# Performance work log

Measured on AMD Instinct MI355X. Metric: run time of the kernel, lower is better.

The kernel has to match this reference:

```python
import jax, jax.numpy as jnp
import numpy as np

B, NEG, NBR, NS, D, T, E = 1024, 5, 50, 1000000, 128, 8, 4
NORM_RATE = 1e-4
NEG_INF = -2.0 ** 32 + 1.0


def leaky(x):
    return jax.nn.leaky_relu(x, 0.01)


def g(x, y):
    # negative squared L2 distance over last dim
    return -jnp.sum((x - y) ** 2, axis=-1)


def setup_inputs():
    key = jax.random.key(0)
    k = jax.random.split(key, 24)
    r_e = float(np.sqrt(3.0 / (NS + D)))
    r_t = float(np.sqrt(3.0 / (D + D)))
    return {
        'e_types': jax.random.randint(k[0], (B,), 0, E),
        's_ids': jax.random.randint(k[1], (B,), 0, NS),
        's_types': jax.random.randint(k[2], (B,), 0, T),
        's_negs': jax.random.randint(k[3], (B, NEG), 0, NS),
        's_nbr_ids': jax.random.randint(k[4], (E, B, NBR), 0, NS),
        's_nbr_masks': jax.random.randint(k[5], (E, B, NBR), 0, 2, dtype=jnp.int32),
        's_nbr_weights': jax.random.uniform(k[6], (E, B, NBR)),
        's_nbr_flags': jax.random.randint(k[7], (E, B, 1), 0, 2, dtype=jnp.int32),
        't_ids': jax.random.randint(k[8], (B,), 0, NS),
        't_types': jax.random.randint(k[9], (B,), 0, T),
        't_negs': jax.random.randint(k[10], (B, NEG), 0, NS),
        't_nbr_ids': jax.random.randint(k[11], (E, B, NBR), 0, NS),
        't_nbr_masks': jax.random.randint(k[12], (E, B, NBR), 0, 2, dtype=jnp.int32),
        't_nbr_weights': jax.random.uniform(k[13], (E, B, NBR)),
        't_nbr_flags': jax.random.randint(k[14], (E, B, 1), 0, 2, dtype=jnp.int32),
        'embedding': jax.random.uniform(k[15], (NS, D), minval=-r_e, maxval=r_e),
        'edge_type_embed': jax.random.uniform(k[16], (E, D), minval=-r_t, maxval=r_t),
        'W_node': jax.random.normal(k[17], (D, D)) * 0.05,
        'b_node': jnp.zeros((D,)),
        'W_nbr': jax.random.normal(k[18], (D, D)) * 0.05,
        'b_nbr': jnp.zeros((D,)),
        'W_att': jax.random.normal(k[19], (D, 1)) * 0.05,
        'b_att': jnp.zeros((1,)),
    }


def _node_latent(emb, W, b, ids):
    # scatter into [n*T, D] then gather at the same unique indices == identity,
    # so this reduces to a gathered linear + leaky_relu.
    return leaky(emb[ids] @ W + b)


def _edge_dist(node_e, ids, e_emb, weight, mask_i, target_e, negs, emb, Wn, bn, Wa, ba):
    # node_e [B,D], ids/weight/mask [B,N], e_emb [D], target_e [B,D], negs [neg,B,D]\n
    mask = mask_i.astype(bool)
    nbr = leaky(emb[ids] @ Wn + bn)                          # [B,N,D]
    d = g(node_e[:, None] + e_emb, nbr)                      # [B,N]
    atts = jax.nn.softmax(jnp.where(mask, d, NEG_INF), axis=-1)
    atts2 = jnp.where(mask, atts, 0.0)
    nw = atts2 * weight                                      # [B,N]
    mutual = g(nbr, target_e[:, None])                       # [B,N]
    mneg = jax.vmap(lambda ne: g(nbr, ne[:, None]))(negs)    # [neg,B,N]
    avg_embed = jnp.einsum('bn,bnd->bd', atts2, nbr)
    nbr_n = jnp.clip(jnp.sum(mask_i.astype(jnp.float32), 1), 1.0, float(NBR))
    ave_w = jnp.sum(weight, 1) / nbr_n                       # [B]
    hete = leaky((ave_w[:, None] * avg_embed) @ Wa + ba)     # [B,1]
    pos = jnp.sum(nw * mutual, -1)                           # [B]
    neg = jnp.sum(nw[None] * mneg, -1)                       # [neg,B]
    return pos, jnp.transpose(neg), hete[:, 0]


def _mutual(node_e, nbr_ids, nbr_masks, nbr_weights, nbr_flags, target_e, negs, emb, ete, Wn, bn, Wa, ba):
    pos, neg, hete = jax.vmap(
        _edge_dist,
        in_axes=(None, 0, 0, 0, 0, None, None, None, None, None, None, None),
    )(node_e, nbr_ids, ete, nbr_weights, nbr_masks, target_e, negs, emb, Wn, bn, Wa, ba)
    # original zeroes the per-type outputs when all flags > 0
    allpos = jnp.all(nbr_flags > 0, axis=(1, 2))             # [E]
    pos = jnp.where(allpos[:, None], 0.0, pos)               # [E,B]
    neg = jnp.where(allpos[:, None, None], 0.0, neg)         # [E,B,neg]
    hete = jnp.where(allpos[:, None], 0.0, hete)             # [E,B]
    mask_et = jnp.transpose(nbr_flags[:, :, 0] > 0)          # [B,E]
    att = jnp.transpose(hete)                                # [B,E]
    att_v1 = jax.nn.softmax(jnp.where(mask_et, att, NEG_INF), axis=1)
    norm_att = jax.nn.softmax(jnp.where(mask_et, att_v1, 0.0), axis=1)
    pos_loss = jnp.sum(norm_att * jnp.transpose(pos), axis=-1)            # [B]
    neg_loss = jnp.einsum('bne,be->bn', jnp.transpose(neg, (1, 2, 0)), norm_att)  # [B,neg]
    return pos_loss, neg_loss


def _forward(e_types, s_ids, s_negs, s_nbr_ids, s_nbr_masks, s_nbr_weights, s_nbr_flags,
             t_ids, t_negs, t_nbr_ids, t_nbr_masks, t_nbr_weights, t_nbr_flags,
             embedding, ete, Wn, bn, Wb, bb, Wa, ba):
    s_e = _node_latent(embedding, Wn, bn, s_ids)             # [B,D]
    t_e = _node_latent(embedding, Wn, bn, t_ids)
    mu = g(s_e + ete[e_types], t_e)                          # [B]
    neg_t = _node_latent(embedding, Wn, bn, t_negs)          # [B,neg,D]
    neg_s = _node_latent(embedding, Wn, bn, s_negs)
    neg_mus_st = g(s_e[:, None], neg_t)                      # [B,neg]
    neg_mus_ts = g(t_e[:, None], neg_s)
    pos_st, neg_st = _mutual(s_e, s_nbr_ids, s_nbr_masks, s_nbr_weights, s_nbr_flags,
                             t_e, jnp.transpose(neg_t, (1, 0, 2)), embedding, ete, Wb, bb, Wa, ba)
    pos_ts, neg_ts = _mutual(t_e, t_nbr_ids, t_nbr_masks, t_nbr_weights, t_nbr_flags,
                             s_e, jnp.transpose(neg_s, (1, 0, 2)), embedding, ete, Wb, bb, Wa, ba)
    lam_pos = mu + pos_st + pos_ts
    loss = (-jnp.mean(jnp.log(jax.nn.sigmoid(lam_pos) + 1e-6))
            - jnp.mean(jnp.log(jax.nn.sigmoid(-(neg_mus_st + neg_st)) + 1e-6))
            - jnp.mean(jnp.log(jax.nn.sigmoid(-(neg_mus_ts + neg_ts)) + 1e-6))
            + NORM_RATE * jnp.sum(ete ** 2))
    return loss


def reference(e_types, s_ids, s_types, s_negs, s_nbr_ids, s_nbr_masks, s_nbr_weights, s_nbr_flags,
              t_ids, t_types, t_negs, t_nbr_ids, t_nbr_masks, t_nbr_weights, t_nbr_flags,
              embedding, edge_type_embed, W_node, b_node, W_nbr, b_nbr, W_att, b_att):
    # s_types/t_types are mathematically inert (scatter/gather cancels); kept for signature fidelity.
    return _forward(e_types, s_ids, s_negs, s_nbr_ids, s_nbr_masks, s_nbr_weights, s_nbr_flags,
                    t_ids, t_negs, t_nbr_ids, t_nbr_masks, t_nbr_weights, t_nbr_flags,
                    embedding, edge_type_embed, W_node, b_node, W_nbr, b_nbr, W_att, b_att)
```

## Files before the change

### kernel.cpp

```cpp
#include <hip/hip_runtime.h>
#include <hip/hip_bf16.h>
#include <cstddef>

#define BN   1024
#define NEGN 5
#define NBRN 50
#define DN   128
#define EN   4
#define MPAD 64
#define NEG_INF_F (-4294967295.0f)

typedef __bf16 bf16_t;
typedef __bf16 bf16x8 __attribute__((ext_vector_type(8)));
typedef __bf16 bf16x4 __attribute__((ext_vector_type(4)));
typedef float  f32x4  __attribute__((ext_vector_type(4)));

__device__ __forceinline__ float leaky_f(float x) { return x >= 0.0f ? x : 0.01f * x; }

__device__ __forceinline__ float wave_sum(float v) {
#pragma unroll
    for (int off = 32; off; off >>= 1) v += __shfl_xor(v, off, 64);
    return v;
}
__device__ __forceinline__ float wave_max(float v) {
#pragma unroll
    for (int off = 32; off; off >>= 1) v = fmaxf(v, __shfl_xor(v, off, 64));
    return v;
}
__device__ __forceinline__ float sigmoid_f(float x) {
    if (x >= 0.0f) { float z = __expf(-x); return 1.0f / (1.0f + z); }
    float z = __expf(x); return z / (1.0f + z);
}

__global__ __launch_bounds__(256) void prep_kernel(
    const float* __restrict__ Wn, bf16_t* __restrict__ WnT)
{
    const int idx = blockIdx.x * 256 + threadIdx.x;
    if (idx < DN * DN) {
        const int n = idx >> 7, k = idx & 127;
        WnT[idx] = (bf16_t)Wn[k * DN + n];
    }
}

__global__ __launch_bounds__(128) void latent_kernel(
    const float* __restrict__ emb, const float* __restrict__ W, const float* __restrict__ bias,
    const int* __restrict__ s_ids, const int* __restrict__ t_ids,
    const int* __restrict__ s_negs, const int* __restrict__ t_negs,
    float* __restrict__ sE, float* __restrict__ tE,
    float* __restrict__ negS, float* __restrict__ negT)
{
    const int tid = threadIdx.x;
    const int r0 = blockIdx.x * 8;
    __shared__ float rows[8][DN];
    __shared__ int ids_l[8];

    if (tid < 8) {
        int r = r0 + tid;
        int id;
        if (r < BN)                       id = s_ids[r];
        else if (r < 2 * BN)              id = t_ids[r - BN];
        else if (r < 2 * BN + BN * NEGN)  id = s_negs[r - 2 * BN];
        else                              id = t_negs[r - 2 * BN - BN * NEGN];
        ids_l[tid] = id;
    }
    __syncthreads();
#pragma unroll
    for (int r8 = 0; r8 < 8; ++r8)
        rows[r8][tid] = emb[(size_t)ids_l[r8] * DN + tid];
    __syncthreads();

    float acc[8];
#pragma unroll
    for (int r8 = 0; r8 < 8; ++r8) acc[r8] = 0.0f;

    for (int i0 = 0; i0 < DN; i0 += 4) {
        const float w0 = W[(i0 + 0) * DN + tid];
        const float w1 = W[(i0 + 1) * DN + tid];
        const float w2 = W[(i0 + 2) * DN + tid];
        const float w3 = W[(i0 + 3) * DN + tid];
#pragma unroll
        for (int r8 = 0; r8 < 8; ++r8) {
            const float4 a = *reinterpret_cast<const float4*>(&rows[r8][i0]);
            acc[r8] = fmaf(a.x, w0, fmaf(a.y, w1, fmaf(a.z, w2, fmaf(a.w, w3, acc[r8]))));
        }
    }
    const float bb = bias[tid];
#pragma unroll
    for (int r8 = 0; r8 < 8; ++r8) {
        const int r = r0 + r8;
        const float v = leaky_f(acc[r8] + bb);
        float* dst;
        if (r < BN)                       dst = sE   + (size_t)r * DN;
        else if (r < 2 * BN)              dst = tE   + (size_t)(r - BN) * DN;
        else if (r < 2 * BN + BN * NEGN)  dst = negS + (size_t)(r - 2 * BN) * DN;
        else                              dst = negT + (size_t)(r - 2 * BN - BN * NEGN) * DN;
        dst[tid] = v;
    }
}

__global__ __launch_bounds__(256, 4) void edge_kernel(
    const float* __restrict__ emb, const float* __restrict__ ete,
    const bf16_t* __restrict__ WnT, const float* __restrict__ bn,
    const float* __restrict__ Wa, const float* __restrict__ ba,
    const int* __restrict__ s_nbr_ids, const int* __restrict__ s_nbr_masks, const float* __restrict__ s_nbr_w,
    const int* __restrict__ t_nbr_ids, const int* __restrict__ t_nbr_masks, const float* __restrict__ t_nbr_w,
    const float* __restrict__ sE, const float* __restrict__ tE,
    const float* __restrict__ negS, const float* __restrict__ negT,
    float* __restrict__ posW, float* __restrict__ heteW, float* __restrict__ negW)
{
    const int bid  = blockIdx.x;
    const int b    = bid & (BN - 1);
    const int e    = (bid >> 10) & 3;
    const int side = bid >> 12;

    const int*   ids_p;  const int* mask_p; const float* w_p;
    const float* node_p; const float* tgt_p; const float* negs_p;
    if (side == 0) { ids_p = s_nbr_ids; mask_p = s_nbr_masks; w_p = s_nbr_w;
                     node_p = sE; tgt_p = tE; negs_p = negT; }
    else           { ids_p = t_nbr_ids; mask_p = t_nbr_masks; w_p = t_nbr_w;
                     node_p = tE; tgt_p = sE; negs_p = negS; }
    const int base = (e * BN + b) * NBRN;

    __shared__ __align__(16) bf16_t buf[MPAD * DN];
    __shared__ __align__(16) bf16_t VT[16 * DN];
    __shared__ float dotL[MPAD][9];
    __shared__ float n2p_l[4][MPAD];
    __shared__ float norm_l[8];

    const int tid  = threadIdx.x;
    const int lane = tid & 63;
    const int w    = tid >> 6;
    const int l15  = lane & 15;
    const int l4   = lane >> 4;

    int   mk_r = 0; float wj_r = 0.0f;
    if (tid < NBRN) { mk_r = mask_p[base + tid]; wj_r = w_p[base + tid]; }

    float4 rg[7];
#pragma unroll
    for (int i = 0; i < 7; ++i) {
        const int flat = i * 256 + tid;
        if (flat < NBRN * 32) {
            const int j = flat >> 5, c4 = flat & 31;
            const int id = ids_p[base + j];
            rg[i] = *reinterpret_cast<const float4*>(emb + (size_t)id * DN + c4 * 4);
        }
    }

    {
        const int q = tid >> 5, c4 = tid & 31;
        const int c = c4 * 4;
        float4 v;
        if (q == 0) {
            const float4 np = *reinterpret_cast<const float4*>(node_p + (size_t)b * DN + c);
            const float4 ep = *reinterpret_cast<const float4*>(ete + e * DN + c);
            v.x = np.x + ep.x; v.y = np.y + ep.y; v.z = np.z + ep.z; v.w = np.w + ep.w;
        } else if (q == 1) {
            v = *reinterpret_cast<const float4*>(tgt_p + (size_t)b * DN + c);
        } else if (q < 7) {
            v = *reinterpret_cast<const float4*>(negs_p + ((size_t)b * NEGN + (q - 2)) * DN + c);
        } else {
            v = *reinterpret_cast<const float4*>(Wa + c);
        }
        float p = v.x * v.x + v.y * v.y + v.z * v.z + v.w * v.w;
#pragma unroll
        for (int off = 1; off <= 16; off <<= 1) p += __shfl_xor(p, off, 64);
        if (c4 == 0) norm_l[q] = p;
        bf16x4 h; h[0]=(bf16_t)v.x; h[1]=(bf16_t)v.y; h[2]=(bf16_t)v.z; h[3]=(bf16_t)v.w;
        *reinterpret_cast<bf16x4*>(&VT[q * DN + (c ^ ((q & 7) << 3))]) = h;
    }

#pragma unroll
    for (int i = 0; i < 7; ++i) {
        const int flat = i * 256 + tid;
        if (flat < NBRN * 32) {
            const int j = flat >> 5, c4 = flat & 31;
            bf16x4 h; h[0]=(bf16_t)rg[i].x; h[1]=(bf16_t)rg[i].y;
                      h[2]=(bf16_t)rg[i].z; h[3]=(bf16_t)rg[i].w;
            *reinterpret_cast<bf16x4*>(&buf[j * DN + ((c4 * 4) ^ ((j & 7) << 3))]) = h;
        }
    }
    __syncthreads();

    bf16x8 bfr[2][4];
#pragma unroll
    for (int ct = 0; ct < 2; ++ct)
#pragma unroll
        for (int ks = 0; ks < 4; ++ks)
            bfr[ct][ks] = *reinterpret_cast<const bf16x8*>(
                WnT + ((2 * w + ct) * 16 + l15) * DN + ks * 32 + l4 * 8);

    f32x4 acc[4][2];
#pragma unroll
    for (int rt = 0; rt < 4; ++rt) {
        acc[rt][0] = (f32x4){0.f, 0.f, 0.f, 0.f};
        acc[rt][1] = (f32x4){0.f, 0.f, 0.f, 0.f};
    }
#pragma unroll
    for (int rt = 0; rt < 4; ++rt) {
        const int row = rt * 16 + l15;
        bf16x8 a[4];
#pragma unroll
        for (int ks = 0; ks < 4; ++ks) {
            const int k0 = ks * 32 + l4 * 8;
            a[ks] = *reinterpret_cast<const bf16x8*>(
                &buf[row * DN + (k0 ^ ((row & 7) << 3))]);
        }
#pragma unroll
        for (int ks = 0; ks < 4; ++ks) {
            acc[rt][0] = __builtin_amdgcn_mfma_f32_16x16x32_bf16(a[ks], bfr[0][ks], acc[rt][0], 0, 0, 0);
            acc[rt][1] = __builtin_amdgcn_mfma_f32_16x16x32_bf16(a[ks], bfr[1][ks], acc[rt][1], 0, 0, 0);
        }
    }

    {
        const float bb0 = bn[(2 * w + 0) * 16 + l15];
        const float bb1 = bn[(2 * w + 1) * 16 + l15];
        const int c0 = (2 * w + 0) * 16 + l15;
        const int c1 = (2 * w + 1) * 16 + l15;
#pragma unroll
        for (int rt = 0; rt < 4; ++rt) {
#pragma unroll
            for (int r = 0; r < 4; ++r) {
                const int row = rt * 16 + l4 * 4 + r;
                const float v0 = leaky_f(acc[rt][0][r] + bb0);
                const float v1 = leaky_f(acc[rt][1][r] + bb1);
                const int sw = (row & 7) << 3;
                buf[row * DN + (c0 ^ sw)] = (bf16_t)v0;
                buf[row * DN + (c1 ^ sw)] = (bf16_t)v1;
                float p = v0 * v0 + v1 * v1;
#pragma unroll
                for (int off = 1; off <= 8; off <<= 1) p += __shfl_xor(p, off, 64);
                if (l15 == 0) n2p_l[w][row] = p;
            }
        }
    }
    __syncthreads();

    {
        f32x4 dacc = (f32x4){0.f, 0.f, 0.f, 0.f};
        const int row = w * 16 + l15;
#pragma unroll
        for (int ks = 0; ks < 4; ++ks) {
            const int k0 = ks * 32 + l4 * 8;
            const bf16x8 a   = *reinterpret_cast<const bf16x8*>(
                &buf[row * DN + (k0 ^ ((row & 7) << 3))]);
            const bf16x8 bfv = *reinterpret_cast<const bf16x8*>(
                &VT[l15 * DN + (k0 ^ ((l15 & 7) << 3))]);
            dacc = __builtin_amdgcn_mfma_f32_16x16x32_bf16(a, bfv, dacc, 0, 0, 0);
        }
        if (l15 < 8) {
#pragma unroll
            for (int r = 0; r < 4; ++r)
                dotL[w * 16 + l4 * 4 + r][l15] = dacc[r];
        }
    }
    __syncthreads();

    if (tid < 64) {
        const int j = tid;
        const bool act = j < NBRN;
        float mut = 0.0f, hw = 0.0f;
        float mn[NEGN];
#pragma unroll
        for (int n = 0; n < NEGN; ++n) mn[n] = 0.0f;
        float x = NEG_INF_F;
        if (act) {
            const float n2 = n2p_l[0][j] + n2p_l[1][j] + n2p_l[2][j] + n2p_l[3][j];
            const float dj = 2.0f * dotL[j][0] - norm_l[0] - n2;
            mut            = 2.0f * dotL[j][1] - norm_l[1] - n2;
#pragma unroll
            for (int n = 0; n < NEGN; ++n) mn[n] = 2.0f * dotL[j][2 + n] - norm_l[2 + n] - n2;
            hw = dotL[j][7];
            x = mk_r ? dj : NEG_INF_F;
        }
        const float m  = wave_max(x);
        const float ex = act ? __expf(x - m) : 0.0f;
        const float S  = wave_sum(ex);
        const float atts  = ex / S;
        const float atts2 = (act && mk_r) ? atts : 0.0f;
        const float nw = atts2 * wj_r;
        const float posv = wave_sum(nw * mut);
        float nsum[NEGN];
#pragma unroll
        for (int n = 0; n < NEGN; ++n) nsum[n] = wave_sum(nw * mn[n]);
        const float wsum = wave_sum(act ? wj_r : 0.0f);
        const float msum = wave_sum(act ? (float)mk_r : 0.0f);
        const float hsum = wave_sum(atts2 * hw);
        if (tid == 0) {
            const float nbr_n = fminf(fmaxf(msum, 1.0f), (float)NBRN);
            const float ave_w = wsum / nbr_n;
            const int o = (side * EN + e) * BN + b;
            posW[o]  = posv;
            heteW[o] = leaky_f(ave_w * hsum + ba[0]);
#pragma unroll
            for (int n = 0; n < NEGN; ++n) negW[(size_t)o * NEGN + n] = nsum[n];
        }
    }
}

__global__ __launch_bounds__(256) void allpos_kernel(
    const int* __restrict__ s_flags, const int* __restrict__ t_flags, int* __restrict__ allpos)
{
    const int side = blockIdx.x >> 2, e = blockIdx.x & 3;
    const int* f = side ? t_flags : s_flags;
    int ok = 1;
    for (int b = threadIdx.x; b < BN; b += 256) ok &= (f[e * BN + b] > 0);
    ok = __syncthreads_and(ok);
    if (threadIdx.x == 0) allpos[blockIdx.x] = ok;
}

__global__ __launch_bounds__(64) void loss_kernel(
    const int* __restrict__ e_types, const float* __restrict__ ete,
    const int* __restrict__ s_flags, const int* __restrict__ t_flags,
    const float* __restrict__ sE, const float* __restrict__ tE,
    const float* __restrict__ negS, const float* __restrict__ negT,
    const float* __restrict__ posW, const float* __restrict__ heteW,
    const float* __restrict__ negW, const int* __restrict__ allpos,
    float* __restrict__ partials)
{
    const int b = blockIdx.x;
    const int lane = threadIdx.x;
    const int et = e_types[b];

    const float se0 = sE[(size_t)b * DN + lane],      se1 = sE[(size_t)b * DN + lane + 64];
    const float te0 = tE[(size_t)b * DN + lane],      te1 = tE[(size_t)b * DN + lane + 64];
    const float ee0 = ete[et * DN + lane],            ee1 = ete[et * DN + lane + 64];

    float d0 = se0 + ee0 - te0, d1 = se1 + ee1 - te1;
    const float mu = -wave_sum(d0 * d0 + d1 * d1);

    float nmst[NEGN], nmts[NEGN];
#pragma unroll
    for (int n = 0; n < NEGN; ++n) {
        const float* nt = negT + ((size_t)b * NEGN + n) * DN;
        const float* ns = negS + ((size_t)b * NEGN + n) * DN;
        float a0 = se0 - nt[lane], a1 = se1 - nt[lane + 64];
        nmst[n] = -wave_sum(a0 * a0 + a1 * a1);
        float c0 = te0 - ns[lane], c1 = te1 - ns[lane + 64];
        nmts[n] = -wave_sum(c0 * c0 + c1 * c1);
    }

    if (lane == 0) {
        float posl[2];
        float negl[2][NEGN];
        for (int side = 0; side < 2; ++side) {
            const int* fl = side ? t_flags : s_flags;
            float att[EN], pv[EN];
            int mk[EN], ap[EN];
#pragma unroll
            for (int ei = 0; ei < EN; ++ei) {
                ap[ei] = allpos[side * EN + ei];
                mk[ei] = fl[ei * BN + b] > 0;
                const int o = (side * EN + ei) * BN + b;
                att[ei] = ap[ei] ? 0.0f : heteW[o];
                pv[ei]  = ap[ei] ? 0.0f : posW[o];
            }
            float x[EN], m = NEG_INF_F;
#pragma unroll
            for (int ei = 0; ei < EN; ++ei) { x[ei] = mk[ei] ? att[ei] : NEG_INF_F; m = fmaxf(m, x[ei]); }
            float s = 0.0f, ex[EN];
#pragma unroll
            for (int ei = 0; ei < EN; ++ei) { ex[ei] = __expf(x[ei] - m); s += ex[ei]; }
            float v1[EN];
#pragma unroll
            for (int ei = 0; ei < EN; ++ei) v1[ei] = ex[ei] / s;
            float y[EN], m2 = NEG_INF_F;
#pragma unroll
            for (int ei = 0; ei < EN; ++ei) { y[ei] = mk[ei] ? v1[ei] : 0.0f; m2 = fmaxf(m2, y[ei]); }
            float s2 = 0.0f, ex2[EN];
#pragma unroll
            for (int ei = 0; ei < EN; ++ei) { ex2[ei] = __expf(y[ei] - m2); s2 += ex2[ei]; }
            float pl = 0.0f;
            float nl[NEGN];
#pragma unroll
            for (int n = 0; n < NEGN; ++n) nl[n] = 0.0f;
#pragma unroll
            for (int ei = 0; ei < EN; ++ei) {
                const float na = ex2[ei] / s2;
                pl += na * pv[ei];
                const int o = (side * EN + ei) * BN + b;
#pragma unroll
                for (int n = 0; n < NEGN; ++n) {
                    const float nv = ap[ei] ? 0.0f : negW[(size_t)o * NEGN + n];
                    nl[n] += na * nv;
                }
            }
            posl[side] = pl;
#pragma unroll
            for (int n = 0; n < NEGN; ++n) negl[side][n] = nl[n];
        }

        const float lam = mu + posl[0] + posl[1];
        float total = -logf(sigmoid_f(lam) + 1e-6f) / (float)BN;
#pragma unroll
        for (int n = 0; n < NEGN; ++n) {
            total += -logf(sigmoid_f(-(nmst[n] + negl[0][n])) + 1e-6f) / (float)(BN * NEGN);
            total += -logf(sigmoid_f(-(nmts[n] + negl[1][n])) + 1e-6f) / (float)(BN * NEGN);
        }
        partials[b] = total;
    }
}

__global__ __launch_bounds__(256) void final_kernel(
    const float* __restrict__ partials, const float* __restrict__ ete, float* __restrict__ out)
{
    __shared__ float red[256];
    const int tid = threadIdx.x;
    float s = 0.0f;
    for (int i = tid; i < BN; i += 256) s += partials[i];
    float t = 0.0f;
    for (int i = tid; i < EN * DN; i += 256) { const float v = ete[i]; t += v * v; }
    red[tid] = s + 1e-4f * t;
    __syncthreads();
    for (int st = 128; st > 0; st >>= 1) {
        if (tid < st) red[tid] += red[tid + st];
        __syncthreads();
    }
    if (tid == 0) out[0] = red[0];
}

extern "C" void kernel_launch(void* const* d_in, const int* in_sizes, int n_in,
                              void* d_out, int out_size, void* d_ws, size_t ws_size,
                              hipStream_t stream)
{
    const int*   e_types   = (const int*)  d_in[0];
    const int*   s_ids     = (const int*)  d_in[1];
    const int*   s_negs    = (const int*)  d_in[3];
    const int*   s_nbr_ids = (const int*)  d_in[4];
    const int*   s_nbr_msk = (const int*)  d_in[5];
    const float* s_nbr_w   = (const float*)d_in[6];
    const int*   s_flags   = (const int*)  d_in[7];
    const int*   t_ids     = (const int*)  d_in[8];
    const int*   t_negs    = (const int*)  d_in[10];
    const int*   t_nbr_ids = (const int*)  d_in[11];
    const int*   t_nbr_msk = (const int*)  d_in[12];
    const float* t_nbr_w   = (const float*)d_in[13];
    const int*   t_flags   = (const int*)  d_in[14];
    const float* emb       = (const float*)d_in[15];
    const float* ete       = (const float*)d_in[16];
    const float* W_node    = (const float*)d_in[17];
    const float* b_node    = (const float*)d_in[18];
    const float* W_nbr     = (const float*)d_in[19];
    const float* b_nbr     = (const float*)d_in[20];
    const float* W_att     = (const float*)d_in[21];
    const float* b_att     = (const float*)d_in[22];

    float* ws   = (float*)d_ws;
    float* sE   = ws;
    float* tE   = sE   + (size_t)BN * DN;
    float* negS = tE   + (size_t)BN * DN;
    float* negT = negS + (size_t)BN * NEGN * DN;
    float* posW = negT + (size_t)BN * NEGN * DN;
    float* heteW= posW + (size_t)2 * EN * BN;
    float* negW = heteW+ (size_t)2 * EN * BN;
    float* parts= negW + (size_t)2 * EN * BN * NEGN;
    int*   apos = (int*)(parts + BN);
    bf16_t* WnT = (bf16_t*)(apos + 8);

    prep_kernel<<<(DN * DN + 255) / 256, 256, 0, stream>>>(W_nbr, WnT);

    latent_kernel<<<(2 * BN + 2 * BN * NEGN) / 8, 128, 0, stream>>>(
        emb, W_node, b_node, s_ids, t_ids, s_negs, t_negs, sE, tE, negS, negT);

    edge_kernel<<<2 * EN * BN, 256, 0, stream>>>(
        emb, ete, WnT, b_nbr, W_att, b_att,
        s_nbr_ids, s_nbr_msk, s_nbr_w,
        t_nbr_ids, t_nbr_msk, t_nbr_w,
        sE, tE, negS, negT, posW, heteW, negW);

    allpos_kernel<<<8, 256, 0, stream>>>(s_flags, t_flags, apos);

    loss_kernel<<<BN, 64, 0, stream>>>(
        e_types, ete, s_flags, t_flags, sE, tE, negS, negT,
        posW, heteW, negW, apos, parts);

    final_kernel<<<1, 256, 0, stream>>>(parts, ete, (float*)d_out);
}
```

Measured before the change: 123.5 us.

## Process both sides per block and prefetch target-side neighbor gather during source compute

```diff
diff --git a/kernel.cpp b/kernel.cpp
--- a/kernel.cpp
+++ b/kernel.cpp
@@ -98,7 +98,7 @@
     }
 }
 
-__global__ __launch_bounds__(256, 4) void edge_kernel(
+__global__ __launch_bounds__(256, 3) void edge_kernel(
     const float* __restrict__ emb, const float* __restrict__ ete,
     const bf16_t* __restrict__ WnT, const float* __restrict__ bn,
     const float* __restrict__ Wa, const float* __restrict__ ba,
@@ -108,24 +108,17 @@
     const float* __restrict__ negS, const float* __restrict__ negT,
     float* __restrict__ posW, float* __restrict__ heteW, float* __restrict__ negW)
 {
-    const int bid  = blockIdx.x;
-    const int b    = bid & (BN - 1);
-    const int e    = (bid >> 10) & 3;
-    const int side = bid >> 12;
-
-    const int*   ids_p;  const int* mask_p; const float* w_p;
-    const float* node_p; const float* tgt_p; const float* negs_p;
-    if (side == 0) { ids_p = s_nbr_ids; mask_p = s_nbr_masks; w_p = s_nbr_w;
-                     node_p = sE; tgt_p = tE; negs_p = negT; }
-    else           { ids_p = t_nbr_ids; mask_p = t_nbr_masks; w_p = t_nbr_w;
-                     node_p = tE; tgt_p = sE; negs_p = negS; }
+    const int bid = blockIdx.x;
+    const int b   = bid & (BN - 1);
+    const int e   = bid >> 10;
     const int base = (e * BN + b) * NBRN;
 
-    __shared__ __align__(16) bf16_t buf[MPAD * DN];
-    __shared__ __align__(16) bf16_t VT[16 * DN];
-    __shared__ float dotL[MPAD][9];
-    __shared__ float n2p_l[4][MPAD];
-    __shared__ float norm_l[8];
+    __shared__ __align__(16) bf16_t bufA[MPAD * DN];
+    __shared__ __align__(16) bf16_t bufB[MPAD * DN];
+    __shared__ __align__(16) bf16_t VT[2][8 * DN];
+    __shared__ float dotL[2][MPAD][9];
+    __shared__ float n2p_l[2][4][MPAD];
+    __shared__ float norm_l[2][8];
 
     const int tid  = threadIdx.x;
     const int lane = tid & 63;
@@ -133,8 +126,9 @@
     const int l15  = lane & 15;
     const int l4   = lane >> 4;
 
-    int   mk_r = 0; float wj_r = 0.0f;
-    if (tid < NBRN) { mk_r = mask_p[base + tid]; wj_r = w_p[base + tid]; }
+    int mk_r = 0; float wj_r = 0.0f;
+    if (w == 0 && lane < NBRN) { mk_r = s_nbr_masks[base + lane]; wj_r = s_nbr_w[base + lane]; }
+    if (w == 1 && lane < NBRN) { mk_r = t_nbr_masks[base + lane]; wj_r = t_nbr_w[base + lane]; }
 
     float4 rg[7];
 #pragma unroll
@@ -142,12 +136,16 @@
         const int flat = i * 256 + tid;
         if (flat < NBRN * 32) {
             const int j = flat >> 5, c4 = flat & 31;
-            const int id = ids_p[base + j];
+            const int id = s_nbr_ids[base + j];
             rg[i] = *reinterpret_cast<const float4*>(emb + (size_t)id * DN + c4 * 4);
         }
     }
 
-    {
+#pragma unroll
+    for (int s = 0; s < 2; ++s) {
+        const float* node_p = s ? tE   : sE;
+        const float* tgt_p  = s ? sE   : tE;
+        const float* negs_p = s ? negS : negT;
         const int q = tid >> 5, c4 = tid & 31;
         const int c = c4 * 4;
         float4 v;
@@ -165,9 +163,9 @@
         float p = v.x * v.x + v.y * v.y + v.z * v.z + v.w * v.w;
 #pragma unroll
         for (int off = 1; off <= 16; off <<= 1) p += __shfl_xor(p, off, 64);
-        if (c4 == 0) norm_l[q] = p;
+        if (c4 == 0) norm_l[s][q] = p;
         bf16x4 h; h[0]=(bf16_t)v.x; h[1]=(bf16_t)v.y; h[2]=(bf16_t)v.z; h[3]=(bf16_t)v.w;
-        *reinterpret_cast<bf16x4*>(&VT[q * DN + (c ^ ((q & 7) << 3))]) = h;
+        *reinterpret_cast<bf16x4*>(&VT[s][q * DN + (c ^ ((q & 7) << 3))]) = h;
     }
 
 #pragma unroll
@@ -177,7 +175,7 @@
             const int j = flat >> 5, c4 = flat & 31;
             bf16x4 h; h[0]=(bf16_t)rg[i].x; h[1]=(bf16_t)rg[i].y;
                       h[2]=(bf16_t)rg[i].z; h[3]=(bf16_t)rg[i].w;
-            *reinterpret_cast<bf16x4*>(&buf[j * DN + ((c4 * 4) ^ ((j & 7) << 3))]) = h;
+            *reinterpret_cast<bf16x4*>(&bufA[j * DN + ((c4 * 4) ^ ((j & 7) << 3))]) = h;
         }
     }
     __syncthreads();
@@ -190,34 +188,49 @@
             bfr[ct][ks] = *reinterpret_cast<const bf16x8*>(
                 WnT + ((2 * w + ct) * 16 + l15) * DN + ks * 32 + l4 * 8);
 
-    f32x4 acc[4][2];
-#pragma unroll
-    for (int rt = 0; rt < 4; ++rt) {
-        acc[rt][0] = (f32x4){0.f, 0.f, 0.f, 0.f};
-        acc[rt][1] = (f32x4){0.f, 0.f, 0.f, 0.f};
-    }
-#pragma unroll
-    for (int rt = 0; rt < 4; ++rt) {
-        const int row = rt * 16 + l15;
-        bf16x8 a[4];
-#pragma unroll
-        for (int ks = 0; ks < 4; ++ks) {
-            const int k0 = ks * 32 + l4 * 8;
-            a[ks] = *reinterpret_cast<const bf16x8*>(
-                &buf[row * DN + (k0 ^ ((row & 7) << 3))]);
-        }
-#pragma unroll
-        for (int ks = 0; ks < 4; ++ks) {
-            acc[rt][0] = __builtin_amdgcn_mfma_f32_16x16x32_bf16(a[ks], bfr[0][ks], acc[rt][0], 0, 0, 0);
-            acc[rt][1] = __builtin_amdgcn_mfma_f32_16x16x32_bf16(a[ks], bfr[1][ks], acc[rt][1], 0, 0, 0);
-        }
-    }
-
-    {
-        const float bb0 = bn[(2 * w + 0) * 16 + l15];
-        const float bb1 = bn[(2 * w + 1) * 16 + l15];
-        const int c0 = (2 * w + 0) * 16 + l15;
-        const int c1 = (2 * w + 1) * 16 + l15;
+#pragma unroll
+    for (int i = 0; i < 7; ++i) {
+        const int flat = i * 256 + tid;
+        if (flat < NBRN * 32) {
+            const int j = flat >> 5, c4 = flat & 31;
+            const int id = t_nbr_ids[base + j];
+            rg[i] = *reinterpret_cast<const float4*>(emb + (size_t)id * DN + c4 * 4);
+        }
+    }
+
+    const float bb0 = bn[(2 * w + 0) * 16 + l15];
+    const float bb1 = bn[(2 * w + 1) * 16 + l15];
+    const int   c0  = (2 * w + 0) * 16 + l15;
+    const int   c1  = (2 * w + 1) * 16 + l15;
+
+#pragma unroll 1
+    for (int s = 0; s < 2; ++s) {
+        bf16_t* buf = s ? bufB : bufA;
+
+        f32x4 acc[4][2];
+#pragma unroll
+        for (int rt = 0; rt < 4; ++rt) {
+            acc[rt][0] = (f32x4){0.f, 0.f, 0.f, 0.f};
+            acc[rt][1] = (f32x4){0.f, 0.f, 0.f, 0.f};
+        }
+#pragma unroll
+        for (int rt = 0; rt < 4; ++rt) {
+            const int row = rt * 16 + l15;
+            bf16x8 a[4];
+#pragma unroll
+            for (int ks = 0; ks < 4; ++ks) {
+                const int k0 = ks * 32 + l4 * 8;
+                a[ks] = *reinterpret_cast<const bf16x8*>(
+                    &buf[row * DN + (k0 ^ ((row & 7) << 3))]);
+            }
+#pragma unroll
+            for (int ks = 0; ks < 4; ++ks) {
+                acc[rt][0] = __builtin_amdgcn_mfma_f32_16x16x32_bf16(a[ks], bfr[0][ks], acc[rt][0], 0, 0, 0);
+                acc[rt][1] = __builtin_amdgcn_mfma_f32_16x16x32_bf16(a[ks], bfr[1][ks], acc[rt][1], 0, 0, 0);
+            }
+        }
+        __syncthreads();
+
 #pragma unroll
         for (int rt = 0; rt < 4; ++rt) {
 #pragma unroll
@@ -231,34 +244,49 @@
                 float p = v0 * v0 + v1 * v1;
 #pragma unroll
                 for (int off = 1; off <= 8; off <<= 1) p += __shfl_xor(p, off, 64);
-                if (l15 == 0) n2p_l[w][row] = p;
-            }
-        }
-    }
-    __syncthreads();
-
-    {
-        f32x4 dacc = (f32x4){0.f, 0.f, 0.f, 0.f};
-        const int row = w * 16 + l15;
-#pragma unroll
-        for (int ks = 0; ks < 4; ++ks) {
-            const int k0 = ks * 32 + l4 * 8;
-            const bf16x8 a   = *reinterpret_cast<const bf16x8*>(
-                &buf[row * DN + (k0 ^ ((row & 7) << 3))]);
-            const bf16x8 bfv = *reinterpret_cast<const bf16x8*>(
-                &VT[l15 * DN + (k0 ^ ((l15 & 7) << 3))]);
-            dacc = __builtin_amdgcn_mfma_f32_16x16x32_bf16(a, bfv, dacc, 0, 0, 0);
-        }
-        if (l15 < 8) {
-#pragma unroll
-            for (int r = 0; r < 4; ++r)
-                dotL[w * 16 + l4 * 4 + r][l15] = dacc[r];
-        }
-    }
-    __syncthreads();
-
-    if (tid < 64) {
-        const int j = tid;
+                if (l15 == 0) n2p_l[s][w][row] = p;
+            }
+        }
+        __syncthreads();
+
+        {
+            f32x4 dacc = (f32x4){0.f, 0.f, 0.f, 0.f};
+            const int row = w * 16 + l15;
+#pragma unroll
+            for (int ks = 0; ks < 4; ++ks) {
+                const int k0 = ks * 32 + l4 * 8;
+                const bf16x8 a = *reinterpret_cast<const bf16x8*>(
+                    &buf[row * DN + (k0 ^ ((row & 7) << 3))]);
+                const int vr = l15 & 7;
+                const bf16x8 bfv = *reinterpret_cast<const bf16x8*>(
+                    &VT[s][vr * DN + (k0 ^ (vr << 3))]);
+                dacc = __builtin_amdgcn_mfma_f32_16x16x32_bf16(a, bfv, dacc, 0, 0, 0);
+            }
+            if (l15 < 8) {
+#pragma unroll
+                for (int r = 0; r < 4; ++r)
+                    dotL[s][w * 16 + l4 * 4 + r][l15] = dacc[r];
+            }
+        }
+
+        if (s == 0) {
+#pragma unroll
+            for (int i = 0; i < 7; ++i) {
+                const int flat = i * 256 + tid;
+                if (flat < NBRN * 32) {
+                    const int j = flat >> 5, c4 = flat & 31;
+                    bf16x4 h; h[0]=(bf16_t)rg[i].x; h[1]=(bf16_t)rg[i].y;
+                              h[2]=(bf16_t)rg[i].z; h[3]=(bf16_t)rg[i].w;
+                    *reinterpret_cast<bf16x4*>(&bufB[j * DN + ((c4 * 4) ^ ((j & 7) << 3))]) = h;
+                }
+            }
+        }
+        __syncthreads();
+    }
+
+    if (w < 2) {
+        const int s = w;
+        const int j = lane;
         const bool act = j < NBRN;
         float mut = 0.0f, hw = 0.0f;
         float mn[NEGN];
@@ -266,12 +294,12 @@
         for (int n = 0; n < NEGN; ++n) mn[n] = 0.0f;
         float x = NEG_INF_F;
         if (act) {
-            const float n2 = n2p_l[0][j] + n2p_l[1][j] + n2p_l[2][j] + n2p_l[3][j];
-            const float dj = 2.0f * dotL[j][0] - norm_l[0] - n2;
-            mut            = 2.0f * dotL[j][1] - norm_l[1] - n2;
-#pragma unroll
-            for (int n = 0; n < NEGN; ++n) mn[n] = 2.0f * dotL[j][2 + n] - norm_l[2 + n] - n2;
-            hw = dotL[j][7];
+            const float n2 = n2p_l[s][0][j] + n2p_l[s][1][j] + n2p_l[s][2][j] + n2p_l[s][3][j];
+            const float dj = 2.0f * dotL[s][j][0] - norm_l[s][0] - n2;
+            mut            = 2.0f * dotL[s][j][1] - norm_l[s][1] - n2;
+#pragma unroll
+            for (int n = 0; n < NEGN; ++n) mn[n] = 2.0f * dotL[s][j][2 + n] - norm_l[s][2 + n] - n2;
+            hw = dotL[s][j][7];
             x = mk_r ? dj : NEG_INF_F;
         }
         const float m  = wave_max(x);
@@ -287,10 +315,10 @@
         const float wsum = wave_sum(act ? wj_r : 0.0f);
         const float msum = wave_sum(act ? (float)mk_r : 0.0f);
         const float hsum = wave_sum(atts2 * hw);
-        if (tid == 0) {
+        if (j == 0) {
             const float nbr_n = fminf(fmaxf(msum, 1.0f), (float)NBRN);
             const float ave_w = wsum / nbr_n;
-            const int o = (side * EN + e) * BN + b;
+            const int o = (s * EN + e) * BN + b;
             posW[o]  = posv;
             heteW[o] = leaky_f(ave_w * hsum + ba[0]);
 #pragma unroll
@@ -463,7 +491,7 @@
     latent_kernel<<<(2 * BN + 2 * BN * NEGN) / 8, 128, 0, stream>>>(
         emb, W_node, b_node, s_ids, t_ids, s_negs, t_negs, sE, tE, negS, negT);
 
-    edge_kernel<<<2 * EN * BN, 256, 0, stream>>>(
+    edge_kernel<<<EN * BN, 256, 0, stream>>>(
         emb, ete, WnT, b_nbr, W_att, b_att,
         s_nbr_ids, s_nbr_msk, s_nbr_w,
         t_nbr_ids, t_nbr_msk, t_nbr_w,
```

New measurement: 140.1 us. 13.5% more time.
